# Performance work log

Measured on AMD Instinct MI355X. Metric: run time of the kernel, lower is better.

Reference implementation:

```python
import jax, jax.numpy as jnp
from jax import lax
import numpy as np

B, Cin, Cout, H, W, K = 8, 128, 128, 64, 64, 3
K2 = K * K
STRIDE, PAD, DIL = 1, 1, 1
EPS = 1e-5


def setup_inputs() -> dict:
    key = jax.random.key(0)
    ks = jax.random.split(key, 9)
    fan_off = Cin * K2
    fan_def = Cin * K2
    x = jax.random.normal(ks[0], (B, Cin, H, W), jnp.float32)
    # small offset weights -> offsets of O(1) pixel, like early training
    offset_w = jax.random.normal(ks[1], (2 * K2, Cin, K, K), jnp.float32) / np.sqrt(fan_off)
    offset_b = 0.01 * jax.random.normal(ks[2], (2 * K2,), jnp.float32)
    deform_w = jax.random.normal(ks[3], (Cout, Cin, K, K), jnp.float32) / np.sqrt(fan_def)
    deform_b = 0.01 * jax.random.normal(ks[4], (Cout,), jnp.float32)
    gamma = 1.0 + 0.1 * jax.random.normal(ks[5], (Cout,), jnp.float32)
    beta = 0.1 * jax.random.normal(ks[6], (Cout,), jnp.float32)
    running_mean = 0.1 * jax.random.normal(ks[7], (Cout,), jnp.float32)
    running_var = jax.random.uniform(ks[8], (Cout,), jnp.float32, 0.5, 1.5)
    return {"x": x, "offset_w": offset_w, "offset_b": offset_b,
            "deform_w": deform_w, "deform_b": deform_b,
            "gamma": gamma, "beta": beta,
            "running_mean": running_mean, "running_var": running_var}


def _deform_block(x, offset_w, offset_b, deform_w, deform_b, gamma, beta, mean, var):
    # 1) offset prediction: standard 3x3 conv -> [B, 2*K2, Ho, Wo]
    offset = lax.conv_general_dilated(
        x, offset_w, window_strides=(STRIDE, STRIDE),
        padding=((PAD, PAD), (PAD, PAD)), rhs_dilation=(DIL, DIL),
        dimension_numbers=("NCHW", "OIHW", "NCHW"))
    offset = offset + offset_b[None, :, None, None]
    Ho, Wo = offset.shape[2], offset.shape[3]

    # torchvision layout: channel 2k -> dy, 2k+1 -> dx for kernel tap k
    off = offset.reshape(B, K2, 2, Ho, Wo)
    dy, dx = off[:, :, 0], off[:, :, 1]              # [B, K2, Ho, Wo]

    ky = (jnp.arange(K2) // K).astype(jnp.float32)
    kx = (jnp.arange(K2) % K).astype(jnp.float32)
    base_y = (jnp.arange(Ho, dtype=jnp.float32) * STRIDE - PAD)[None, :] + (ky * DIL)[:, None]  # [K2, Ho]
    base_x = (jnp.arange(Wo, dtype=jnp.float32) * STRIDE - PAD)[None, :] + (kx * DIL)[:, None]  # [K2, Wo]
    py = base_y[None, :, :, None] + dy               # [B, K2, Ho, Wo]
    px = base_x[None, :, None, :] + dx

    # 2) bilinear sampling with zero padding outside the image
    y0 = jnp.floor(py)
    x0 = jnp.floor(px)
    wy1 = py - y0; wy0 = 1.0 - wy1
    wx1 = px - x0; wx0 = 1.0 - wx1
    y0i = y0.astype(jnp.int32)
    x0i = x0.astype(jnp.int32)
    xf = x.reshape(B, Cin, H * W)

    def corner(yi, xi, wgt):
        valid = (yi >= 0) & (yi < H) & (xi >= 0) & (xi < W)
        idx = (jnp.clip(yi, 0, H - 1) * W + jnp.clip(xi, 0, W - 1)).reshape(B, 1, -1)
        g = jnp.take_along_axis(xf, idx, axis=2).reshape(B, Cin, K2, Ho, Wo)
        return g * (wgt * valid)[:, None]

    samp = (corner(y0i, x0i, wy0 * wx0)
            + corner(y0i, x0i + 1, wy0 * wx1)
            + corner(y0i + 1, x0i, wy1 * wx0)
            + corner(y0i + 1, x0i + 1, wy1 * wx1))   # [B, Cin, K2, Ho, Wo]

    # 3) conv-like accumulation over (Cin, K2)
    out = jnp.einsum("bckhw,ock->bohw", samp, deform_w.reshape(Cout, Cin, K2))
    out = out + deform_b[None, :, None, None]

    # 4) BatchNorm (inference, running stats) + SiLU
    scale = gamma / jnp.sqrt(var + EPS)
    out = (out - mean[None, :, None, None]) * scale[None, :, None, None] + beta[None, :, None, None]
    return out * jax.nn.sigmoid(out)


def reference(x, offset_w, offset_b, deform_w, deform_b, gamma, beta, running_mean, running_var):
    return _deform_block(x, offset_w, offset_b, deform_w, deform_b,
                         gamma, beta, running_mean, running_var)
```

## Files before the change

kernel.cpp:

```cpp
#include <hip/hip_runtime.h>

typedef float f32x4 __attribute__((ext_vector_type(4)));
typedef __bf16 bf16x8 __attribute__((ext_vector_type(8)));
typedef unsigned short u16x8 __attribute__((ext_vector_type(8)));

static constexpr int B_ = 8, Cin = 128, Cout = 128, K2 = 9;
static constexpr int HW  = 64 * 64;
static constexpr int CHW = Cin * HW;
static constexpr int KC  = Cin * K2;
static constexpr int SLD = 136;

static __device__ __forceinline__ unsigned short f2bf(float f) {
  unsigned int u = __builtin_bit_cast(unsigned int, f);
  u = u + 0x7fffu + ((u >> 16) & 1u);
  return (unsigned short)(u >> 16);
}
static __device__ __forceinline__ float b2f_lo(unsigned int u) {
  return __builtin_bit_cast(float, u << 16);
}
static __device__ __forceinline__ float b2f_hi(unsigned int u) {
  return __builtin_bit_cast(float, u & 0xffff0000u);
}

__global__ __launch_bounds__(256) void prep_trans_kernel(
    const float* __restrict__ x, const float* __restrict__ dw,
    const float* __restrict__ ow, unsigned short* __restrict__ wsW2,
    unsigned short* __restrict__ wOffB2, unsigned short* __restrict__ xt) {
  int bid = blockIdx.x;
  int t = threadIdx.x;

  int swz = (bid & 7) * 64 + (bid >> 3);
  int b = swz >> 6, y = swz & 63;
  int lane = t & 63, cq = t >> 6;
  __shared__ unsigned short L[64 * SLD];
  const float* xb = x + b * CHW + y * 64;
#pragma unroll
  for (int i = 0; i < 32; ++i) {
    int c = i * 4 + cq;
    L[lane * SLD + c] = f2bf(xb[c * HW + lane]);
  }
  __syncthreads();
  int p = t >> 2, q = t & 3;
  unsigned short* op = xt + (size_t)b * HW * 128 + y * 64 * 128 + p * 128 + q * 32;
#pragma unroll
  for (int s = 0; s < 4; ++s)
    *(u16x8*)(op + s * 8) = *(const u16x8*)&L[p * SLD + q * 32 + s * 8];

  for (int i = bid * 256 + t; i < 8 * 9 * 4 * 512; i += 512 * 256) {
    int j = i & 7, ln = (i >> 3) & 63, ks = (i >> 9) & 3, t2 = i >> 11;
    int k = t2 % 9, w = t2 / 9;
    int oc = w * 16 + (ln & 15);
    int c = ks * 32 + (ln >> 4) * 8 + j;
    wsW2[i] = f2bf(dw[(oc * Cin + c) * K2 + k]);
  }
  {
    int i = bid * 256 + t;
    if (i < 9 * 4 * 2 * 512) {
      int j = i & 7, ln = (i >> 3) & 63, m = (i >> 9) & 1, t3 = i >> 10;
      int ks = t3 & 3, r = t3 >> 2;
      int oc = m * 16 + (ln & 15);
      int c = ks * 32 + (ln >> 4) * 8 + j;
      wOffB2[i] = (oc < 18) ? f2bf(ow[(oc * Cin + c) * K2 + r]) : (unsigned short)0;
    }
  }
}

__global__ __launch_bounds__(512, 4) void fused_kernel(
    const unsigned short* __restrict__ xt, const unsigned short* __restrict__ wsW2,
    const unsigned short* __restrict__ wOffB2, const float* __restrict__ ob,
    const float* __restrict__ dbias, const float* __restrict__ gamma,
    const float* __restrict__ beta, const float* __restrict__ mean,
    const float* __restrict__ var, float* __restrict__ out) {
  int bid = blockIdx.x;
  int swz = (bid & 7) * 64 + (bid >> 3);
  int b = swz >> 6, ho = swz & 63;
  int t = threadIdx.x;
  int lane = t & 63, wv = t >> 6;
  int pos = lane;
  int col = lane & 15, g = lane >> 4;

  __shared__ unsigned short SAB[2][64 * SLD];
  __shared__ float T[64 * 20];
  __shared__ float RW4[576 * 4];
  __shared__ unsigned RI[576];

  const unsigned short* xtb = xt + (size_t)b * HW * 128;
  const unsigned int* xtb32 = (const unsigned int*)xtb;

  f32x4 accO[2];
  accO[0] = (f32x4){0.f, 0.f, 0.f, 0.f};
  accO[1] = (f32x4){0.f, 0.f, 0.f, 0.f};

  auto stageA = [&](int r, int buf) {
    int ky = r / 3, kx = r % 3;
    int yv = ho + ky - 1, xc = pos + kx - 1;
    bool ok = ((unsigned)yv < 64u) && ((unsigned)xc < 64u);
    int yc = min(max(yv, 0), 63), xcc = min(max(xc, 0), 63);
    const unsigned short* qq = xtb + (yc * 64 + xcc) * 128 + wv * 16;
#pragma unroll
    for (int i = 0; i < 2; ++i) {
      u16x8 sm = *(const u16x8*)(qq + i * 8);
      if (!ok) sm = (u16x8){0, 0, 0, 0, 0, 0, 0, 0};
      *(u16x8*)&SAB[buf][pos * SLD + wv * 16 + i * 8] = sm;
    }
  };

  stageA(0, 0);
  __syncthreads();
  for (int r = 0; r < 9; ++r) {
    int cur = r & 1;
    if (r < 8) stageA(r + 1, cur ^ 1);
    if (wv < 4) {
#pragma unroll
      for (int ks = 0; ks < 4; ++ks) {
        bf16x8 bfr = *(const bf16x8*)&SAB[cur][(wv * 16 + col) * SLD + ks * 32 + g * 8];
        u16x8 af0 = *(const u16x8*)(wOffB2 + ((r * 4 + ks) * 2 + 0) * 512 + lane * 8);
        u16x8 af1 = *(const u16x8*)(wOffB2 + ((r * 4 + ks) * 2 + 1) * 512 + lane * 8);
        accO[0] = __builtin_amdgcn_mfma_f32_16x16x32_bf16(
            __builtin_bit_cast(bf16x8, af0), bfr, accO[0], 0, 0, 0);
        accO[1] = __builtin_amdgcn_mfma_f32_16x16x32_bf16(
            __builtin_bit_cast(bf16x8, af1), bfr, accO[1], 0, 0, 0);
      }
    }
    __syncthreads();
  }
  if (wv < 4) {
#pragma unroll
    for (int m = 0; m < 2; ++m)
#pragma unroll
      for (int rg = 0; rg < 4; ++rg) {
        int row = m * 16 + g * 4 + rg;
        if (row < 18) T[(wv * 16 + col) * 20 + row] = accO[m][rg] + ob[row];
      }
  }
  __syncthreads();

#pragma unroll
  for (int it = 0; it < 2; ++it) {
    int idx = it * 64 + lane;
    if (idx < 72) {
      int k = idx >> 3, rr = idx & 7;
      int pp = wv * 8 + rr;
      float dy = T[pp * 20 + 2 * k], dx = T[pp * 20 + 2 * k + 1];
      float py = (float)(ho - 1 + k / 3) + dy;
      float px = (float)(pp - 1 + k % 3) + dx;
      float y0f = floorf(py), x0f = floorf(px);
      float wy1 = py - y0f, wy0 = 1.f - wy1;
      float wx1 = px - x0f, wx0 = 1.f - wx1;
      int y0 = (int)y0f, x0 = (int)x0f;
      bool vy0 = (unsigned)y0 < 64u, vy1 = (unsigned)(y0 + 1) < 64u;
      bool vx0 = (unsigned)x0 < 64u, vx1 = (unsigned)(x0 + 1) < 64u;
      float w00 = (vy0 && vx0) ? wy0 * wx0 : 0.f;
      float w01 = (vy0 && vx1) ? wy0 * wx1 : 0.f;
      float w10 = (vy1 && vx0) ? wy1 * wx0 : 0.f;
      float w11 = (vy1 && vx1) ? wy1 * wx1 : 0.f;
      int y0c = min(max(y0, 0), 63), y1c = min(max(y0 + 1, 0), 63);
      int xb2 = min(max(x0, 0), 62);
      unsigned pkw = (unsigned)(y0c * 64 + xb2) | ((unsigned)(y1c * 64 + xb2) << 12);
      if (x0 == 63) pkw |= (1u << 24);
      if (x0 == -1) pkw |= (1u << 25);
      int ridx = k * 64 + pp;
      RW4[ridx * 4 + 0] = w00; RW4[ridx * 4 + 1] = w01;
      RW4[ridx * 4 + 2] = w10; RW4[ridx * 4 + 3] = w11;
      RI[ridx] = pkw;
    }
  }
  __syncthreads();

  f32x4 acc[4];
#pragma unroll
  for (int j = 0; j < 4; ++j) acc[j] = (f32x4){0.f, 0.f, 0.f, 0.f};
  const unsigned short* wA = wsW2 + wv * (9 * 4 * 512) + lane * 8;

  {
#pragma unroll
    for (int r = 0; r < 8; ++r) {
      int pp = wv * 8 + r, ridx = pp;
      unsigned pk = RI[ridx];
      int o0 = pk & 4095, o1 = (pk >> 12) & 4095;
      bool s0 = (pk >> 24) & 1, s1 = (pk >> 25) & 1;
      const unsigned int* r0 = xtb32 + o0 * 64;
      const unsigned int* r1 = xtb32 + o1 * 64;
      unsigned c00 = r0[lane], c01 = r0[lane + 64];
      unsigned c10 = r1[lane], c11 = r1[lane + 64];
      unsigned a0 = s0 ? c01 : c00, a1 = s1 ? c00 : c01;
      unsigned a2 = s0 ? c11 : c10, a3 = s1 ? c10 : c11;
      float wx = RW4[ridx * 4], wy = RW4[ridx * 4 + 1];
      float wz = RW4[ridx * 4 + 2], ww = RW4[ridx * 4 + 3];
      float lo = wx * b2f_lo(a0) + wy * b2f_lo(a1) + wz * b2f_lo(a2) + ww * b2f_lo(a3);
      float hi = wx * b2f_hi(a0) + wy * b2f_hi(a1) + wz * b2f_hi(a2) + ww * b2f_hi(a3);
      *(unsigned*)&SAB[0][pp * SLD + 2 * lane] =
          ((unsigned)f2bf(lo)) | (((unsigned)f2bf(hi)) << 16);
    }
  }
  __syncthreads();

  for (int k = 0; k < 9; ++k) {
    int cur = k & 1;
    unsigned c00[8], c01[8], c10[8], c11[8];
    if (k < 8) {
#pragma unroll
      for (int r = 0; r < 8; ++r) {
        int ridx = (k + 1) * 64 + wv * 8 + r;
        unsigned pk = RI[ridx];
        int o0 = pk & 4095, o1 = (pk >> 12) & 4095;
        const unsigned int* r0 = xtb32 + o0 * 64;
        const unsigned int* r1 = xtb32 + o1 * 64;
        c00[r] = r0[lane]; c01[r] = r0[lane + 64];
        c10[r] = r1[lane]; c11[r] = r1[lane + 64];
      }
    }
    u16x8 af[4];
#pragma unroll
    for (int ks = 0; ks < 4; ++ks)
      af[ks] = *(const u16x8*)(wA + (k * 4 + ks) * 512);
#pragma unroll
    for (int pt = 0; pt < 4; ++pt)
#pragma unroll
      for (int ks = 0; ks < 4; ++ks) {
        bf16x8 bfr = *(const bf16x8*)&SAB[cur][(pt * 16 + col) * SLD + ks * 32 + g * 8];
        acc[pt] = __builtin_amdgcn_mfma_f32_16x16x32_bf16(
            __builtin_bit_cast(bf16x8, af[ks]), bfr, acc[pt], 0, 0, 0);
      }
    if (k < 8) {
#pragma unroll
      for (int r = 0; r < 8; ++r) {
        int ridx = (k + 1) * 64 + wv * 8 + r;
        unsigned pk = RI[ridx];
        bool s0 = (pk >> 24) & 1, s1 = (pk >> 25) & 1;
        float wx = RW4[ridx * 4], wy = RW4[ridx * 4 + 1];
        float wz = RW4[ridx * 4 + 2], ww = RW4[ridx * 4 + 3];
        unsigned a0 = s0 ? c01[r] : c00[r], a1 = s1 ? c00[r] : c01[r];
        unsigned a2 = s0 ? c11[r] : c10[r], a3 = s1 ? c10[r] : c11[r];
        float lo = wx * b2f_lo(a0) + wy * b2f_lo(a1) + wz * b2f_lo(a2) + ww * b2f_lo(a3);
        float hi = wx * b2f_hi(a0) + wy * b2f_hi(a1) + wz * b2f_hi(a2) + ww * b2f_hi(a3);
        *(unsigned*)&SAB[cur ^ 1][(wv * 8 + r) * SLD + 2 * lane] =
            ((unsigned)f2bf(lo)) | (((unsigned)f2bf(hi)) << 16);
      }
    }
    __syncthreads();
  }

  float* op = out + b * (Cout * HW) + ho * 64;
  int ocb = wv * 16 + g * 4;
#pragma unroll
  for (int r = 0; r < 4; ++r) {
    int oc = ocb + r;
    float sc = gamma[oc] * rsqrtf(var[oc] + 1e-5f);
    float bs = beta[oc] - mean[oc] * sc;
    float db = dbias[oc];
#pragma unroll
    for (int pt = 0; pt < 4; ++pt) {
      float v = (acc[pt][r] + db) * sc + bs;
      op[oc * HW + pt * 16 + col] = v / (1.f + __expf(-v));
    }
  }
}

extern "C" void kernel_launch(void* const* d_in, const int* in_sizes, int n_in,
                              void* d_out, int out_size, void* d_ws, size_t ws_size,
                              hipStream_t stream) {
  const float* x     = (const float*)d_in[0];
  const float* ow    = (const float*)d_in[1];
  const float* ob    = (const float*)d_in[2];
  const float* dw    = (const float*)d_in[3];
  const float* db    = (const float*)d_in[4];
  const float* gamma = (const float*)d_in[5];
  const float* beta  = (const float*)d_in[6];
  const float* mean  = (const float*)d_in[7];
  const float* var   = (const float*)d_in[8];

  char* wsc = (char*)d_ws;
  unsigned short* wsW2   = (unsigned short*)wsc;
  unsigned short* wOffB2 = (unsigned short*)(wsc + 294912);
  unsigned short* xt     = (unsigned short*)(wsc + 368640);

  prep_trans_kernel<<<512, 256, 0, stream>>>(x, dw, ow, wsW2, wOffB2, xt);
  fused_kernel<<<512, 512, 0, stream>>>(xt, wsW2, wOffB2, ob, db, gamma, beta,
                                        mean, var, (float*)d_out);
}
```

Baseline: 56.69 us.

## Spread offset-conv MFMA across all eight waves and use packed bf16 conversion

The offset-prediction GEMM previously ran on only four of eight waves, each doing two M-tiles. It now gives each of the eight waves one (M,N) tile, which halves the MFMA chain per wave and removes the idle-wave imbalance. The A-stage load is rewritten as per-lane 32-bit row loads, RW4 weights are read as one float4, and the manual bf16 rounding is replaced by the hardware v_cvt_pk_bf16_f32 instruction. The narrower staging loads may raise the load instruction count, and the hardware conversion may round slightly differently from the manual routine.

```diff
diff --git a/kernel.cpp b/kernel.cpp
--- a/kernel.cpp
+++ b/kernel.cpp
@@ -20,6 +20,11 @@
 }
 static __device__ __forceinline__ float b2f_hi(unsigned int u) {
   return __builtin_bit_cast(float, u & 0xffff0000u);
+}
+static __device__ __forceinline__ unsigned cvt_pk_bf16(float lo, float hi) {
+  unsigned r;
+  asm("v_cvt_pk_bf16_f32 %0, %1, %2" : "=v"(r) : "v"(lo), "v"(hi));
+  return r;
 }
 
 __global__ __launch_bounds__(256) void prep_trans_kernel(
@@ -76,7 +81,6 @@
   int b = swz >> 6, ho = swz & 63;
   int t = threadIdx.x;
   int lane = t & 63, wv = t >> 6;
-  int pos = lane;
   int col = lane & 15, g = lane >> 4;
 
   __shared__ unsigned short SAB[2][64 * SLD];
@@ -87,51 +91,45 @@
   const unsigned short* xtb = xt + (size_t)b * HW * 128;
   const unsigned int* xtb32 = (const unsigned int*)xtb;
 
-  f32x4 accO[2];
-  accO[0] = (f32x4){0.f, 0.f, 0.f, 0.f};
-  accO[1] = (f32x4){0.f, 0.f, 0.f, 0.f};
-
   auto stageA = [&](int r, int buf) {
     int ky = r / 3, kx = r % 3;
-    int yv = ho + ky - 1, xc = pos + kx - 1;
-    bool ok = ((unsigned)yv < 64u) && ((unsigned)xc < 64u);
-    int yc = min(max(yv, 0), 63), xcc = min(max(xc, 0), 63);
-    const unsigned short* qq = xtb + (yc * 64 + xcc) * 128 + wv * 16;
-#pragma unroll
-    for (int i = 0; i < 2; ++i) {
-      u16x8 sm = *(const u16x8*)(qq + i * 8);
-      if (!ok) sm = (u16x8){0, 0, 0, 0, 0, 0, 0, 0};
-      *(u16x8*)&SAB[buf][pos * SLD + wv * 16 + i * 8] = sm;
+    int yv = ho + ky - 1;
+    bool oky = (unsigned)yv < 64u;
+    int yc = min(max(yv, 0), 63);
+#pragma unroll
+    for (int rr = 0; rr < 8; ++rr) {
+      int p = wv * 8 + rr;
+      int xc = p + kx - 1;
+      bool ok = oky && ((unsigned)xc < 64u);
+      int xcc = min(max(xc, 0), 63);
+      unsigned v = ok ? xtb32[(yc * 64 + xcc) * 64 + lane] : 0u;
+      *(unsigned*)&SAB[buf][p * SLD + 2 * lane] = v;
     }
   };
+
+  f32x4 accO = (f32x4){0.f, 0.f, 0.f, 0.f};
+  int mA = wv >> 2, nA = wv & 3;
 
   stageA(0, 0);
   __syncthreads();
   for (int r = 0; r < 9; ++r) {
     int cur = r & 1;
     if (r < 8) stageA(r + 1, cur ^ 1);
-    if (wv < 4) {
-#pragma unroll
-      for (int ks = 0; ks < 4; ++ks) {
-        bf16x8 bfr = *(const bf16x8*)&SAB[cur][(wv * 16 + col) * SLD + ks * 32 + g * 8];
-        u16x8 af0 = *(const u16x8*)(wOffB2 + ((r * 4 + ks) * 2 + 0) * 512 + lane * 8);
-        u16x8 af1 = *(const u16x8*)(wOffB2 + ((r * 4 + ks) * 2 + 1) * 512 + lane * 8);
-        accO[0] = __builtin_amdgcn_mfma_f32_16x16x32_bf16(
-            __builtin_bit_cast(bf16x8, af0), bfr, accO[0], 0, 0, 0);
-        accO[1] = __builtin_amdgcn_mfma_f32_16x16x32_bf16(
-            __builtin_bit_cast(bf16x8, af1), bfr, accO[1], 0, 0, 0);
-      }
+#pragma unroll
+    for (int ks = 0; ks < 4; ++ks) {
+      bf16x8 bfr = *(const bf16x8*)&SAB[cur][(nA * 16 + col) * SLD + ks * 32 + g * 8];
+      u16x8 af = *(const u16x8*)(wOffB2 + ((r * 4 + ks) * 2 + mA) * 512 + lane * 8);
+      accO = __builtin_amdgcn_mfma_f32_16x16x32_bf16(
+          __builtin_bit_cast(bf16x8, af), bfr, accO, 0, 0, 0);
     }
     __syncthreads();
   }
-  if (wv < 4) {
-#pragma unroll
-    for (int m = 0; m < 2; ++m)
-#pragma unroll
-      for (int rg = 0; rg < 4; ++rg) {
-        int row = m * 16 + g * 4 + rg;
-        if (row < 18) T[(wv * 16 + col) * 20 + row] = accO[m][rg] + ob[row];
-      }
+  {
+#pragma unroll
+    for (int rg = 0; rg < 4; ++rg) {
+      int row = mA * 16 + g * 4 + rg;
+      if (row < 18) T[(nA * 16 + col) * 20 + row] = accO[rg] + ob[row];
+    }
   }
   __syncthreads();
 
@@ -185,12 +183,10 @@
       unsigned c10 = r1[lane], c11 = r1[lane + 64];
       unsigned a0 = s0 ? c01 : c00, a1 = s1 ? c00 : c01;
       unsigned a2 = s0 ? c11 : c10, a3 = s1 ? c10 : c11;
-      float wx = RW4[ridx * 4], wy = RW4[ridx * 4 + 1];
-      float wz = RW4[ridx * 4 + 2], ww = RW4[ridx * 4 + 3];
-      float lo = wx * b2f_lo(a0) + wy * b2f_lo(a1) + wz * b2f_lo(a2) + ww * b2f_lo(a3);
-      float hi = wx * b2f_hi(a0) + wy * b2f_hi(a1) + wz * b2f_hi(a2) + ww * b2f_hi(a3);
-      *(unsigned*)&SAB[0][pp * SLD + 2 * lane] =
-          ((unsigned)f2bf(lo)) | (((unsigned)f2bf(hi)) << 16);
+      float4 wv4 = *(const float4*)&RW4[ridx * 4];
+      float lo = wv4.x * b2f_lo(a0) + wv4.y * b2f_lo(a1) + wv4.z * b2f_lo(a2) + wv4.w * b2f_lo(a3);
+      float hi = wv4.x * b2f_hi(a0) + wv4.y * b2f_hi(a1) + wv4.z * b2f_hi(a2) + wv4.w * b2f_hi(a3);
+      *(unsigned*)&SAB[0][pp * SLD + 2 * lane] = cvt_pk_bf16(lo, hi);
     }
   }
   __syncthreads();
@@ -228,14 +224,12 @@
         int ridx = (k + 1) * 64 + wv * 8 + r;
         unsigned pk = RI[ridx];
         bool s0 = (pk >> 24) & 1, s1 = (pk >> 25) & 1;
-        float wx = RW4[ridx * 4], wy = RW4[ridx * 4 + 1];
-        float wz = RW4[ridx * 4 + 2], ww = RW4[ridx * 4 + 3];
+        float4 wv4 = *(const float4*)&RW4[ridx * 4];
         unsigned a0 = s0 ? c01[r] : c00[r], a1 = s1 ? c00[r] : c01[r];
         unsigned a2 = s0 ? c11[r] : c10[r], a3 = s1 ? c10[r] : c11[r];
-        float lo = wx * b2f_lo(a0) + wy * b2f_lo(a1) + wz * b2f_lo(a2) + ww * b2f_lo(a3);
-        float hi = wx * b2f_hi(a0) + wy * b2f_hi(a1) + wz * b2f_hi(a2) + ww * b2f_hi(a3);
-        *(unsigned*)&SAB[cur ^ 1][(wv * 8 + r) * SLD + 2 * lane] =
-            ((unsigned)f2bf(lo)) | (((unsigned)f2bf(hi)) << 16);
+        float lo = wv4.x * b2f_lo(a0) + wv4.y * b2f_lo(a1) + wv4.z * b2f_lo(a2) + wv4.w * b2f_lo(a3);
+        float hi = wv4.x * b2f_hi(a0) + wv4.y * b2f_hi(a1) + wv4.z * b2f_hi(a2) + wv4.w * b2f_hi(a3);
+        *(unsigned*)&SAB[cur ^ 1][(wv * 8 + r) * SLD + 2 * lane] = cvt_pk_bf16(lo, hi);
       }
     }
     __syncthreads();
```

After: 51.50 us. -9.1%, faster.
